# Kernel tuning notes

Hardware: AMD Instinct MI355X
Metric: run time of the kernel (lower is better)

Reference implementation:

```python
import jax, jax.numpy as jnp
import numpy as np
import math

V, D, H, F, L, S, B = 50257, 1024, 16, 4096, 4, 2048, 2
DK = D // H

def setup_inputs() -> dict:
    key = jax.random.key(0)
    ks = iter(jax.random.split(key, 32))
    std = 0.02
    def nrm(shape):
        return (std * jax.random.normal(next(ks), shape)).astype(jnp.float32)
    inp = {
        "x": jax.random.randint(next(ks), (B, S), 0, V, dtype=jnp.int32),
        "emb": nrm((V, D)),
        "ln1_g": jnp.ones((L, D), jnp.float32), "ln1_b": jnp.zeros((L, D), jnp.float32),
        "wq": nrm((L, D, D)), "wk": nrm((L, D, D)), "wv": nrm((L, D, D)), "wo": nrm((L, D, D)),
        "ln2_g": jnp.ones((L, D), jnp.float32), "ln2_b": jnp.zeros((L, D), jnp.float32),
        "w1": nrm((L, D, F)), "b1": jnp.zeros((L, F), jnp.float32),
        "w2": nrm((L, F, D)), "b2": jnp.zeros((L, D), jnp.float32),
        "lnf_g": jnp.ones((D,), jnp.float32), "lnf_b": jnp.zeros((D,), jnp.float32),
        "head_w": nrm((D, V)), "head_b": jnp.zeros((V,), jnp.float32),
    }
    return inp

def _layernorm(x, g, b, eps=1e-5):
    mu = jnp.mean(x, axis=-1, keepdims=True)
    var = jnp.var(x, axis=-1, keepdims=True)
    return (x - mu) * jax.lax.rsqrt(var + eps) * g + b

def _posenc(seq_len, d_model, dtype):
    pos = jnp.arange(seq_len, dtype=jnp.float32)[:, None]                  # [S,1]
    div = jnp.exp(jnp.arange(0, d_model, 2, dtype=jnp.float32) * (-math.log(10000.0) / d_model))
    ang = pos * div                                                        # [S,D/2]
    pe = jnp.stack([jnp.sin(ang), jnp.cos(ang)], axis=-1).reshape(seq_len, d_model)
    return pe.astype(dtype)

def reference(x, emb, ln1_g, ln1_b, wq, wk, wv, wo, ln2_g, ln2_b, w1, b1, w2, b2, lnf_g, lnf_b, head_w, head_b):
    b, s = x.shape
    h = emb[x] + _posenc(s, D, emb.dtype)[None]                            # [B,S,D]
    causal = jnp.tril(jnp.ones((s, s), dtype=bool))                       # True = keep
    scale = 1.0 / math.sqrt(DK)
    neg_inf = jnp.finfo(h.dtype).min
    for l in range(L):
        # --- attention sublayer ---
        hn = _layernorm(h, ln1_g[l], ln1_b[l])
        q = (hn @ wq[l]).reshape(b, s, H, DK)
        k = (hn @ wk[l]).reshape(b, s, H, DK)
        v = (hn @ wv[l]).reshape(b, s, H, DK)
        scores = jnp.einsum("bqhd,bkhd->bhqk", q, k) * scale
        scores = jnp.where(causal[None, None], scores, neg_inf)
        w = jax.nn.softmax(scores, axis=-1)
        attn = jnp.einsum("bhqk,bkhd->bqhd", w, v).reshape(b, s, D)
        h = h + attn @ wo[l]
        # --- FFN sublayer ---
        hn = _layernorm(h, ln2_g[l], ln2_b[l])
        h = h + jax.nn.relu(hn @ w1[l] + b1[l]) @ w2[l] + b2[l]
    h = _layernorm(h, lnf_g, lnf_b)
    logits = h @ head_w + head_b                                           # [B,S,V]
    return logits
```

## Files before the change

### kernel.cpp

```cpp
#include <hip/hip_runtime.h>
#include <math.h>

#define VOCAB 50257
#define VPAD  50432
#define DM    1024
#define NH    16
#define DKH   64
#define FF    4096
#define NL    4
#define SEQ   2048
#define BATCH 2
#define MROWS (BATCH*SEQ)

typedef __bf16 bf16_t;
typedef __bf16 bf16x8 __attribute__((ext_vector_type(8)));
typedef __bf16 bf16x4 __attribute__((ext_vector_type(4)));
typedef float  f32x4  __attribute__((ext_vector_type(4)));

typedef void as1_void __attribute__((address_space(1)));
typedef void as3_void __attribute__((address_space(3)));

__device__ __forceinline__ void gload_lds16(const void* g, void* l) {
  __builtin_amdgcn_global_load_lds((as1_void*)g, (as3_void*)l, 16, 0, 0);
}

__device__ __forceinline__ uint32_t lds_addr32(const void* p) {
  return (uint32_t)(uintptr_t)(as3_void*)p;
}

__device__ __forceinline__ bf16x8 dsr128(uint32_t addr) {
  bf16x8 v;
  asm volatile("ds_read_b128 %0, %1" : "=v"(v) : "v"(addr));
  return v;
}

#define FENCE asm volatile("" ::: "memory")
#define BAR() do { FENCE; __builtin_amdgcn_s_barrier(); FENCE; } while (0)
#define LGKM0_FENCE() do { \
  asm volatile("s_waitcnt lgkmcnt(0)" ::: "memory"); \
  __builtin_amdgcn_sched_barrier(0); \
} while (0)

__global__ __launch_bounds__(256) void embed_kernel(const int* __restrict__ x,
    const float* __restrict__ emb, float* __restrict__ h) {
  int row = blockIdx.x;
  int s = row & (SEQ - 1);
  int d = threadIdx.x * 4;
  const float* e = emb + (size_t)x[row] * DM + d;
  float4 v = *(const float4*)e;
  float vin[4] = {v.x, v.y, v.z, v.w};
  float out[4];
#pragma unroll
  for (int j = 0; j < 4; ++j) {
    int dd = d + j;
    int i = dd >> 1;
    float freq = expf(-0.017988946039016376f * (float)i);
    float ang = (float)s * freq;
    float pe = (dd & 1) ? cosf(ang) : sinf(ang);
    out[j] = vin[j] + pe;
  }
  *(float4*)(h + (size_t)row * DM + d) = make_float4(out[0], out[1], out[2], out[3]);
}

__global__ __launch_bounds__(256) void ln_kernel(const float* __restrict__ x,
    const float* __restrict__ g, const float* __restrict__ b, bf16_t* __restrict__ out) {
  int row = blockIdx.x;
  int tid = threadIdx.x, lane = tid & 63, wave = tid >> 6;
  const float* xr = x + (size_t)row * DM;
  float4 v = ((const float4*)xr)[tid];
  float s1 = v.x + v.y + v.z + v.w;
  float s2 = v.x * v.x + v.y * v.y + v.z * v.z + v.w * v.w;
#pragma unroll
  for (int d = 1; d < 64; d <<= 1) { s1 += __shfl_xor(s1, d); s2 += __shfl_xor(s2, d); }
  __shared__ float red[8];
  if (lane == 0) { red[wave] = s1; red[4 + wave] = s2; }
  __syncthreads();
  s1 = red[0] + red[1] + red[2] + red[3];
  s2 = red[4] + red[5] + red[6] + red[7];
  float mu = s1 * (1.0f / DM);
  float var = s2 * (1.0f / DM) - mu * mu;
  float rs = rsqrtf(var + 1e-5f);
  float4 gv = ((const float4*)g)[tid];
  float4 bv = ((const float4*)b)[tid];
  bf16x4 o;
  o[0] = (bf16_t)((v.x - mu) * rs * gv.x + bv.x);
  o[1] = (bf16_t)((v.y - mu) * rs * gv.y + bv.y);
  o[2] = (bf16_t)((v.z - mu) * rs * gv.z + bv.z);
  o[3] = (bf16_t)((v.w - mu) * rs * gv.w + bv.w);
  *(bf16x4*)(out + (size_t)row * DM + tid * 4) = o;
}

__global__ __launch_bounds__(256) void transpose_cast_kernel(const float* __restrict__ in,
    bf16_t* __restrict__ out, int K, int N, int Npad) {
  __shared__ float tile[32][33];
  int n0 = blockIdx.x * 32, k0 = blockIdx.y * 32;
  int tx = threadIdx.x & 31, ty = threadIdx.x >> 5;
#pragma unroll
  for (int kk = ty; kk < 32; kk += 8) {
    int n = n0 + tx;
    tile[kk][tx] = (n < N) ? in[(size_t)(k0 + kk) * N + n] : 0.f;
  }
  __syncthreads();
#pragma unroll
  for (int nn = ty; nn < 32; nn += 8) {
    out[(size_t)(n0 + nn) * K + k0 + tx] = (bf16_t)tile[tx][nn];
  }
}

__global__ __launch_bounds__(256) void wtrans_kernel(
    const float* __restrict__ wq, const float* __restrict__ wk,
    const float* __restrict__ wv, const float* __restrict__ wo,
    const float* __restrict__ w1, const float* __restrict__ w2,
    bf16_t* __restrict__ qkvT, bf16_t* __restrict__ woT,
    bf16_t* __restrict__ w1T, bf16_t* __restrict__ w2T) {
  int id = blockIdx.x;
  const float* src; bf16_t* dst; int K, N, tk, tn;
  if (id < 4096) {
    int m = id >> 10, tile_i = id & 1023;
    tk = tile_i >> 5; tn = tile_i & 31; K = 1024; N = 1024;
    src = (m == 0) ? wq : (m == 1) ? wk : (m == 2) ? wv : wo;
    dst = (m < 3) ? qkvT + (size_t)m * DM * DM : woT;
  } else if (id < 8192) {
    int tile_i = id - 4096;
    tk = tile_i >> 7; tn = tile_i & 127; K = 1024; N = 4096;
    src = w1; dst = w1T;
  } else {
    int tile_i = id - 8192;
    tk = tile_i >> 5; tn = tile_i & 31; K = 4096; N = 1024;
    src = w2; dst = w2T;
  }
  __shared__ float tile[32][33];
  int n0 = tn * 32, k0 = tk * 32;
  int tx = threadIdx.x & 31, ty = threadIdx.x >> 5;
#pragma unroll
  for (int kk = ty; kk < 32; kk += 8)
    tile[kk][tx] = src[(size_t)(k0 + kk) * N + n0 + tx];
  __syncthreads();
#pragma unroll
  for (int nn = ty; nn < 32; nn += 8)
    dst[(size_t)(n0 + nn) * K + k0 + tx] = (bf16_t)tile[tx][nn];
}

__global__ __launch_bounds__(256) void vtrans_kernel(const bf16_t* __restrict__ qkv,
    bf16_t* __restrict__ vT) {
  int sb = blockIdx.x, hh = blockIdx.y, bb = blockIdx.z;
  __shared__ bf16_t t[64][72];
  int tid = threadIdx.x;
  const bf16_t* src = qkv + ((size_t)bb * SEQ + sb * 64) * (3 * DM) + 2 * DM + hh * DKH;
#pragma unroll
  for (int c = 0; c < 2; ++c) {
    int u = c * 256 + tid;
    int s = u >> 3, d8 = u & 7;
    *(bf16x8*)&t[s][d8 * 8] = *(const bf16x8*)(src + (size_t)s * (3 * DM) + d8 * 8);
  }
  __syncthreads();
  bf16_t* dst = vT + ((size_t)(bb * NH + hh) * DKH) * SEQ + sb * 64;
#pragma unroll
  for (int c = 0; c < 2; ++c) {
    int u = c * 256 + tid;
    int dk = u >> 3, s8 = u & 7;
    bf16x8 v;
#pragma unroll
    for (int j = 0; j < 8; ++j) v[j] = t[s8 * 8 + j][dk];
    *(bf16x8*)(dst + (size_t)dk * SEQ + s8 * 8) = v;
  }
}

__global__ __launch_bounds__(256, 2) void gemm128_kernel(
    const bf16_t* __restrict__ A, const bf16_t* __restrict__ Bt, int K,
    const float* __restrict__ bias, const float* __restrict__ Rsd,
    float* Cf, bf16_t* Cb, int ldc, int Nvalid, int relu, int gridM, int gridN) {
  __shared__ __align__(16) bf16_t lds[32768];

  int nwg = gridM * gridN;
  int orig = blockIdx.x;
  int q = nwg >> 3, rr = nwg & 7;
  int xcd = orig & 7, idx = orig >> 3;
  int swz = (xcd < rr ? xcd * (q + 1) : rr * (q + 1) + (xcd - rr) * q) + idx;
  int bm = swz % gridM, bn = swz / gridM;
  int m0 = bm * 128, n0 = bn * 128;

  int tid = threadIdx.x, lane = tid & 63, wave = tid >> 6;
  int g = lane >> 4, r = lane & 15;
  int wr = wave >> 1, wc = wave & 1;

  f32x4 zero = {0.f, 0.f, 0.f, 0.f};
  f32x4 acc[4][4];
#pragma unroll
  for (int i = 0; i < 4; ++i)
#pragma unroll
    for (int j = 0; j < 4; ++j) acc[i][j] = zero;

  const bf16_t* Abase = A + (size_t)m0 * K;
  const bf16_t* Bbase = Bt + (size_t)n0 * K;
  int NT = K >> 6;

  uint32_t L0 = lds_addr32(lds);
  uint32_t aF = L0 + (uint32_t)((g * 128 + wr * 64 + r) * 16);
  uint32_t bF = L0 + 32768u + (uint32_t)((g * 128 + wc * 64 + r) * 16);

  auto stage = [&](int t) {
    int b = t & 1, k0 = t << 6;
    bf16_t* dA = lds + (size_t)b * 8192;
    bf16_t* dB = lds + 16384 + (size_t)b * 8192;
#pragma unroll
    for (int j = 0; j < 4; ++j) {
      int u = j * 256 + tid;
      int row = u & 127, k8 = u >> 7;
      gload_lds16(Abase + (size_t)row * K + k0 + k8 * 8, dA + (j * 256 + wave * 64) * 8);
    }
#pragma unroll
    for (int j = 0; j < 4; ++j) {
      int u = j * 256 + tid;
      int row = u & 127, k8 = u >> 7;
      gload_lds16(Bbase + (size_t)row * K + k0 + k8 * 8, dB + (j * 256 + wave * 64) * 8);
    }
  };

  stage(0);
  if (NT > 1) {
    stage(1);
    asm volatile("s_waitcnt vmcnt(8)" ::: "memory");
  } else {
    asm volatile("s_waitcnt vmcnt(0)" ::: "memory");
  }
  BAR();

  for (int t = 0; t < NT; ++t) {
    uint32_t boff = (uint32_t)((t & 1) << 14);
    bf16x8 af[4][2], bfr[4][2];
#pragma unroll
    for (int mr = 0; mr < 4; ++mr)
#pragma unroll
      for (int kk = 0; kk < 2; ++kk)
        af[mr][kk] = dsr128(aF + boff + (uint32_t)(kk * 8192 + mr * 256));
#pragma unroll
    for (int nr = 0; nr < 4; ++nr)
#pragma unroll
      for (int kk = 0; kk < 2; ++kk)
        bfr[nr][kk] = dsr128(bF + boff + (uint32_t)(kk * 8192 + nr * 256));
    LGKM0_FENCE();
    BAR();
    if (t + 2 < NT) stage(t + 2);
    __builtin_amdgcn_s_setprio(1);
#pragma unroll
    for (int mr = 0; mr < 4; ++mr)
#pragma unroll
      for (int nr = 0; nr < 4; ++nr) {
        acc[mr][nr] = __builtin_amdgcn_mfma_f32_16x16x32_bf16(af[mr][0], bfr[nr][0], acc[mr][nr], 0, 0, 0);
        acc[mr][nr] = __builtin_amdgcn_mfma_f32_16x16x32_bf16(af[mr][1], bfr[nr][1], acc[mr][nr], 0, 0, 0);
      }
    __builtin_amdgcn_s_setprio(0);
    __builtin_amdgcn_sched_barrier(0);
    if (t + 2 < NT) {
      asm volatile("s_waitcnt vmcnt(8)" ::: "memory");
    } else {
      asm volatile("s_waitcnt vmcnt(0)" ::: "memory");
    }
    BAR();
  }

#pragma unroll
  for (int mr = 0; mr < 4; ++mr) {
    int row = m0 + wr * 64 + mr * 16 + g * 4;
#pragma unroll
    for (int nr = 0; nr < 4; ++nr) {
      int col = n0 + wc * 64 + nr * 16 + r;
      if (col < Nvalid) {
        float bval = bias ? bias[col] : 0.f;
#pragma unroll
        for (int i = 0; i < 4; ++i) {
          float vv = acc[mr][nr][i] + bval;
          if (relu) vv = fmaxf(vv, 0.f);
          size_t idxo = (size_t)(row + i) * ldc + col;
          if (Rsd) vv += Rsd[idxo];
          if (Cf) Cf[idxo] = vv;
          if (Cb) Cb[idxo] = (bf16_t)vv;
        }
      }
    }
  }
}

__global__ __launch_bounds__(512, 2) void gemm256_kernel(
    const bf16_t* __restrict__ A, const bf16_t* __restrict__ Bt, int K,
    const float* __restrict__ bias, float* Cf, bf16_t* Cb,
    int ldc, int Nvalid, int relu, int gridM, int gridN) {
  __shared__ __align__(16) bf16_t lds[65536];

  int nwg = gridM * gridN;
  int orig = blockIdx.x;
  int q = nwg >> 3, rr = nwg & 7;
  int xcd = orig & 7, idx = orig >> 3;
  int swz = (xcd < rr ? xcd * (q + 1) : rr * (q + 1) + (xcd - rr) * q) + idx;
  int bm = swz % gridM, bn = swz / gridM;
  int m0 = bm * 256, n0 = bn * 256;

  int tid = threadIdx.x, lane = tid & 63, wave = tid >> 6;
  int g = lane >> 4, r = lane & 15;
  int wr = wave >> 2, wc = wave & 3;

  f32x4 zero = {0.f, 0.f, 0.f, 0.f};
  f32x4 acc[8][4];
#pragma unroll
  for (int i = 0; i < 8; ++i)
#pragma unroll
    for (int j = 0; j < 4; ++j) acc[i][j] = zero;

  const bf16_t* Ab = A + (size_t)m0 * K;
  const bf16_t* Bb = Bt + (size_t)n0 * K;
  int NT = K >> 6;

  uint32_t L0 = lds_addr32(lds);
  uint32_t laneOff = (uint32_t)(g * 2048 + r * 16);
  uint32_t aBase0 = L0 + ((uint32_t)wr << 14) + laneOff;
  uint32_t bBase0 = L0 + 65536u + ((uint32_t)(wc >> 1) << 14) + laneOff
                  + (uint32_t)((wc & 1) * 1024);

  auto stageA = [&](int t, int hh) {
    int b = t & 1, k0 = t << 6;
    const bf16_t* src = Ab + (size_t)(hh * 128) * K + k0;
    bf16_t* dst = lds + (size_t)(b * 2 + hh) * 8192;
#pragma unroll
    for (int j = 0; j < 2; ++j) {
      int u = j * 512 + tid;
      gload_lds16(src + (size_t)(u & 127) * K + (u >> 7) * 8, dst + (j * 512 + wave * 64) * 8);
    }
  };
  auto stageB = [&](int t, int hh) {
    int b = t & 1, k0 = t << 6;
    const bf16_t* src = Bb + (size_t)(hh * 128) * K + k0;
    bf16_t* dst = lds + 32768 + (size_t)(b * 2 + hh) * 8192;
#pragma unroll
    for (int j = 0; j < 2; ++j) {
      int u = j * 512 + tid;
      gload_lds16(src + (size_t)(u & 127) * K + (u >> 7) * 8, dst + (j * 512 + wave * 64) * 8);
    }
  };

  stageB(0, 0); stageB(0, 1); stageA(0, 0); stageA(0, 1);
  if (NT > 1) {
    stageB(1, 0); stageB(1, 1);
    asm volatile("s_waitcnt vmcnt(4)" ::: "memory");
  } else {
    asm volatile("s_waitcnt vmcnt(0)" ::: "memory");
  }
  BAR();

  for (int t = 0; t < NT; ++t) {
    uint32_t bsel = (uint32_t)((t & 1) << 15);
    uint32_t Aaddr = aBase0 + bsel;
    uint32_t Baddr = bBase0 + bsel;

    bf16x8 a0[4][2], a1[4][2], b01[2][2], b23[2][2];

#pragma unroll
    for (int mi = 0; mi < 4; ++mi)
#pragma unroll
      for (int kk = 0; kk < 2; ++kk)
        a0[mi][kk] = dsr128(Aaddr + (uint32_t)(kk * 8192 + mi * 256));
#pragma unroll
    for (int ni = 0; ni < 2; ++ni)
#pragma unroll
      for (int kk = 0; kk < 2; ++kk)
        b01[ni][kk] = dsr128(Baddr + (uint32_t)(kk * 8192 + ni * 256));
    if (t + 1 < NT) stageA(t + 1, 0);
    BAR();
    LGKM0_FENCE();
    __builtin_amdgcn_s_setprio(1);
#pragma unroll
    for (int mi = 0; mi < 4; ++mi)
#pragma unroll
      for (int ni = 0; ni < 2; ++ni)
#pragma unroll
        for (int kk = 0; kk < 2; ++kk)
          acc[mi][ni] = __builtin_amdgcn_mfma_f32_16x16x32_bf16(a0[mi][kk], b01[ni][kk], acc[mi][ni], 0, 0, 0);
    __builtin_amdgcn_s_setprio(0);
    __builtin_amdgcn_sched_barrier(0);
    BAR();

#pragma unroll
    for (int ni = 0; ni < 2; ++ni)
#pragma unroll
      for (int kk = 0; kk < 2; ++kk)
        b23[ni][kk] = dsr128(Baddr + (uint32_t)(kk * 8192 + (ni + 2) * 256));
    if (t + 1 < NT) stageA(t + 1, 1);
    BAR();
    LGKM0_FENCE();
    __builtin_amdgcn_s_setprio(1);
#pragma unroll
    for (int mi = 0; mi < 4; ++mi)
#pragma unroll
      for (int ni = 0; ni < 2; ++ni)
#pragma unroll
        for (int kk = 0; kk < 2; ++kk)
          acc[mi][ni + 2] = __builtin_amdgcn_mfma_f32_16x16x32_bf16(a0[mi][kk], b23[ni][kk], acc[mi][ni + 2], 0, 0, 0);
    __builtin_amdgcn_s_setprio(0);
    __builtin_amdgcn_sched_barrier(0);
    BAR();

#pragma unroll
    for (int mi = 0; mi < 4; ++mi)
#pragma unroll
      for (int kk = 0; kk < 2; ++kk)
        a1[mi][kk] = dsr128(Aaddr + (uint32_t)(kk * 8192 + (mi + 4) * 256));
    if (t + 2 < NT) stageB(t + 2, 0);
    BAR();
    LGKM0_FENCE();
    __builtin_amdgcn_s_setprio(1);
#pragma unroll
    for (int mi = 0; mi < 4; ++mi)
#pragma unroll
      for (int ni = 0; ni < 2; ++ni)
#pragma unroll
        for (int kk = 0; kk < 2; ++kk)
          acc[mi + 4][ni] = __builtin_amdgcn_mfma_f32_16x16x32_bf16(a1[mi][kk], b01[ni][kk], acc[mi + 4][ni], 0, 0, 0);
    __builtin_amdgcn_s_setprio(0);
    __builtin_amdgcn_sched_barrier(0);
    BAR();

    if (t + 2 < NT) stageB(t + 2, 1);
    __builtin_amdgcn_sched_barrier(0);
    __builtin_amdgcn_s_setprio(1);
#pragma unroll
    for (int mi = 0; mi < 4; ++mi)
#pragma unroll
      for (int ni = 0; ni < 2; ++ni)
#pragma unroll
        for (int kk = 0; kk < 2; ++kk)
          acc[mi + 4][ni + 2] = __builtin_amdgcn_mfma_f32_16x16x32_bf16(a1[mi][kk], b23[ni][kk], acc[mi + 4][ni + 2], 0, 0, 0);
    __builtin_amdgcn_s_setprio(0);
    __builtin_amdgcn_sched_barrier(0);
    if (t + 2 < NT) {
      asm volatile("s_waitcnt vmcnt(4)" ::: "memory");
    } else {
      asm volatile("s_waitcnt vmcnt(0)" ::: "memory");
    }
    BAR();
  }

#pragma unroll
  for (int mi = 0; mi < 8; ++mi) {
    int row = m0 + wr * 128 + mi * 16 + g * 4;
#pragma unroll
    for (int ni = 0; ni < 4; ++ni) {
      int col = n0 + wc * 64 + ni * 16 + r;
      if (col < Nvalid) {
        float bval = bias ? bias[col] : 0.f;
#pragma unroll
        for (int i = 0; i < 4; ++i) {
          float vv = acc[mi][ni][i] + bval;
          if (relu) vv = fmaxf(vv, 0.f);
          size_t idxo = (size_t)(row + i) * ldc + col;
          if (Cf) Cf[idxo] = vv;
          if (Cb) Cb[idxo] = (bf16_t)vv;
        }
      }
    }
  }
}

__global__ __launch_bounds__(512, 4) void gemmhd_kernel(
    const bf16_t* __restrict__ A, const bf16_t* __restrict__ Bt, int K,
    const float* __restrict__ bias, float* __restrict__ Cf,
    int ldc, int Nvalid, int gridM, int gridN) {
  __shared__ __align__(16) bf16_t lds[24576];

  int nwg = gridM * gridN;
  int orig = blockIdx.x;
  int q = nwg >> 3, rr = nwg & 7;
  int xcd = orig & 7, idx = orig >> 3;
  int swz = (xcd < rr ? xcd * (q + 1) : rr * (q + 1) + (xcd - rr) * q) + idx;
  int bm = swz % gridM, bn = swz / gridM;
  int m0 = bm * 128, n0 = bn * 256;

  int tid = threadIdx.x, lane = tid & 63, wave = tid >> 6;
  int g = lane >> 4, r = lane & 15;
  int wr = wave >> 2, wc = wave & 3;

  f32x4 zero = {0.f, 0.f, 0.f, 0.f};
  f32x4 acc[4][4];
#pragma unroll
  for (int i = 0; i < 4; ++i)
#pragma unroll
    for (int j = 0; j < 4; ++j) acc[i][j] = zero;

  const bf16_t* Abase = A + (size_t)m0 * K;
  const bf16_t* Bbase = Bt + (size_t)n0 * K;
  int NT = K >> 5;

  uint32_t L0 = lds_addr32(lds);
  uint32_t aF = L0 + (uint32_t)(g * 2048 + (wr * 64 + r) * 16);
  uint32_t bF = L0 + 16384u + (uint32_t)(g * 4096 + (wc * 64 + r) * 16);

  auto stage = [&](int t) {
    int b = t & 1, k0 = t << 5;
    bf16_t* dA = lds + (size_t)b * 4096;
    bf16_t* dB = lds + 8192 + (size_t)b * 8192;
    {
      int u = tid;
      int row = u & 127, k8 = u >> 7;
      gload_lds16(Abase + (size_t)row * K + k0 + k8 * 8, dA + (wave * 64) * 8);
    }
#pragma unroll
    for (int j = 0; j < 2; ++j) {
      int u = j * 512 + tid;
      int row = u & 255, k8 = u >> 8;
      gload_lds16(Bbase + (size_t)row * K + k0 + k8 * 8, dB + (j * 512 + wave * 64) * 8);
    }
  };

  stage(0);
  if (NT > 1) {
    stage(1);
    asm volatile("s_waitcnt vmcnt(3)" ::: "memory");
  } else {
    asm volatile("s_waitcnt vmcnt(0)" ::: "memory");
  }
  BAR();

  for (int t = 0; t < NT; ++t) {
    uint32_t aoff = (uint32_t)((t & 1) << 13);
    uint32_t boff = (uint32_t)((t & 1) << 14);
    bf16x8 af[4], bfr[4];
#pragma unroll
    for (int mr = 0; mr < 4; ++mr) af[mr] = dsr128(aF + aoff + (uint32_t)(mr * 256));
#pragma unroll
    for (int nr = 0; nr < 4; ++nr) bfr[nr] = dsr128(bF + boff + (uint32_t)(nr * 256));
    LGKM0_FENCE();
    BAR();
    if (t + 2 < NT) stage(t + 2);
    __builtin_amdgcn_s_setprio(1);
#pragma unroll
    for (int mr = 0; mr < 4; ++mr)
#pragma unroll
      for (int nr = 0; nr < 4; ++nr)
        acc[mr][nr] = __builtin_amdgcn_mfma_f32_16x16x32_bf16(af[mr], bfr[nr], acc[mr][nr], 0, 0, 0);
    __builtin_amdgcn_s_setprio(0);
    __builtin_amdgcn_sched_barrier(0);
    if (t + 2 < NT) {
      asm volatile("s_waitcnt vmcnt(3)" ::: "memory");
    } else {
      asm volatile("s_waitcnt vmcnt(0)" ::: "memory");
    }
    BAR();
  }

#pragma unroll
  for (int mr = 0; mr < 4; ++mr) {
    int row = m0 + wr * 64 + mr * 16 + g * 4;
#pragma unroll
    for (int nr = 0; nr < 4; ++nr) {
      int col = n0 + wc * 64 + nr * 16 + r;
      if (col < Nvalid) {
        float bval = bias ? bias[col] : 0.f;
#pragma unroll
        for (int i = 0; i < 4; ++i) {
          Cf[(size_t)(row + i) * ldc + col] = acc[mr][nr][i] + bval;
        }
      }
    }
  }
}

__global__ __launch_bounds__(512, 4) void attn_kernel(const bf16_t* __restrict__ Qg,
    const bf16_t* __restrict__ Kg, const bf16_t* __restrict__ vT, bf16_t* __restrict__ Og,
    int ldq) {
  int bq = (int)gridDim.x - 1 - (int)blockIdx.x;
  int hh = blockIdx.y, bb = blockIdx.z;
  int tid = threadIdx.x, lane = tid & 63, wave = tid >> 6;
  int g = lane >> 4, r = lane & 15;
  __shared__ __align__(16) bf16_t Kl[2][4096];
  __shared__ __align__(16) bf16_t Vl[2][4096];
  __shared__ __align__(16) bf16_t Pl[8][1024];

  size_t base = (size_t)bb * SEQ * ldq + hh * DKH;
  size_t vbase = ((size_t)(bb * NH + hh)) * DKH * SEQ;
  size_t baseO = (size_t)bb * SEQ * DM + hh * DKH;
  int q0 = bq * 128 + wave * 16;
  const bf16_t* qrowp = Qg + base + (size_t)(q0 + r) * ldq;
  bf16x8 qf0 = *(const bf16x8*)(qrowp + g * 8);
  bf16x8 qf1 = *(const bf16x8*)(qrowp + 32 + g * 8);
#pragma unroll
  for (int j = 0; j < 8; ++j) {
    qf0[j] = (bf16_t)((float)qf0[j] * 0.125f);
    qf1[j] = (bf16_t)((float)qf1[j] * 0.125f);
  }

  uint32_t KlA = lds_addr32(&Kl[0][0]);
  uint32_t VlA = lds_addr32(&Vl[0][0]);
  int slot0 = g ^ (r & 7), slot1 = (4 + g) ^ (r & 7);

  f32x4 zero = {0.f, 0.f, 0.f, 0.f};
  f32x4 accO[4];
#pragma unroll
  for (int dt = 0; dt < 4; ++dt) accO[dt] = zero;
  float m_i[4], l_i[4];
#pragma unroll
  for (int i = 0; i < 4; ++i) { m_i[i] = -1e30f; l_i[i] = 0.f; }

  int skv = tid >> 3, kslot = tid & 7, kdk8 = kslot ^ (skv & 7);
  int sdk = tid >> 3, vslot = tid & 7, vkv8 = vslot ^ (sdk & 7);
  const bf16_t* ksrc0 = Kg + base + (size_t)skv * ldq + kdk8 * 8;
  const bf16_t* vsrc0 = vT + vbase + (size_t)sdk * SEQ + vkv8 * 8;

  auto stage = [&](int kb) {
    int c = kb & 1;
    gload_lds16(ksrc0 + (size_t)(kb * 64) * ldq, &Kl[c][(wave * 64) * 8]);
    gload_lds16(vsrc0 + kb * 64, &Vl[c][(wave * 64) * 8]);
  };

  int nkb = 2 * bq + 2;
  stage(0); stage(1);
  asm volatile("s_waitcnt vmcnt(2)" ::: "memory");
  BAR();

  for (int kb = 0; kb < nkb; ++kb) {
    uint32_t koff = KlA + (uint32_t)((kb & 1) << 13);
    uint32_t voff = VlA + (uint32_t)((kb & 1) << 13);

    bf16x8 kf[4][2];
#pragma unroll
    for (int ct = 0; ct < 4; ++ct) {
      int kvrow = ct * 16 + r;
      kf[ct][0] = dsr128(koff + (uint32_t)((kvrow * 8 + slot0) * 16));
      kf[ct][1] = dsr128(koff + (uint32_t)((kvrow * 8 + slot1) * 16));
    }
    LGKM0_FENCE();
    f32x4 sc[4];
#pragma unroll
    for (int ct = 0; ct < 4; ++ct) {
      f32x4 s = zero;
      s = __builtin_amdgcn_mfma_f32_16x16x32_bf16(qf0, kf[ct][0], s, 0, 0, 0);
      s = __builtin_amdgcn_mfma_f32_16x16x32_bf16(qf1, kf[ct][1], s, 0, 0, 0);
      sc[ct] = s;
    }

    bool full = (kb * 64 + 63) <= q0;
#pragma unroll
    for (int i = 0; i < 4; ++i) {
      float mx = m_i[i];
      if (full) {
#pragma unroll
        for (int ct = 0; ct < 4; ++ct) mx = fmaxf(mx, sc[ct][i]);
      } else {
        int qglob = q0 + g * 4 + i;
#pragma unroll
        for (int ct = 0; ct < 4; ++ct) {
          int kglob = kb * 64 + ct * 16 + r;
          float s = (kglob <= qglob) ? sc[ct][i] : -1e30f;
          sc[ct][i] = s;
          mx = fmaxf(mx, s);
        }
      }
#pragma unroll
      for (int d = 1; d < 16; d <<= 1) mx = fmaxf(mx, __shfl_xor(mx, d));
      float scl = __expf(m_i[i] - mx);
      l_i[i] *= scl;
      m_i[i] = mx;
      float rsum = 0.f;
#pragma unroll
      for (int ct = 0; ct < 4; ++ct) {
        float p = __expf(sc[ct][i] - mx);
        sc[ct][i] = p;
        rsum += p;
      }
#pragma unroll
      for (int d = 1; d < 16; d <<= 1) rsum += __shfl_xor(rsum, d);
      l_i[i] += rsum;
#pragma unroll
      for (int dt = 0; dt < 4; ++dt) accO[dt][i] *= scl;
    }

#pragma unroll
    for (int ct = 0; ct < 4; ++ct) {
      int kcol = ct * 16 + r;
#pragma unroll
      for (int i = 0; i < 4; ++i)
        Pl[wave][((kcol >> 3) * 16 + g * 4 + i) * 8 + (kcol & 7)] = (bf16_t)sc[ct][i];
    }
    bf16x8 pa0 = *(const bf16x8*)&Pl[wave][((0 + g) * 16 + r) * 8];
    bf16x8 pa1 = *(const bf16x8*)&Pl[wave][((4 + g) * 16 + r) * 8];

    bf16x8 vb[4][2];
#pragma unroll
    for (int dt = 0; dt < 4; ++dt) {
      int dkrow = dt * 16 + r;
      vb[dt][0] = dsr128(voff + (uint32_t)((dkrow * 8 + slot0) * 16));
      vb[dt][1] = dsr128(voff + (uint32_t)((dkrow * 8 + slot1) * 16));
    }
    LGKM0_FENCE();
#pragma unroll
    for (int dt = 0; dt < 4; ++dt) {
      accO[dt] = __builtin_amdgcn_mfma_f32_16x16x32_bf16(pa0, vb[dt][0], accO[dt], 0, 0, 0);
      accO[dt] = __builtin_amdgcn_mfma_f32_16x16x32_bf16(pa1, vb[dt][1], accO[dt], 0, 0, 0);
    }

    BAR();
    if (kb + 2 < nkb) {
      stage(kb + 2);
      asm volatile("s_waitcnt vmcnt(2)" ::: "memory");
    } else {
      asm volatile("s_waitcnt vmcnt(0)" ::: "memory");
    }
    BAR();
  }

#pragma unroll
  for (int dt = 0; dt < 4; ++dt)
#pragma unroll
    for (int i = 0; i < 4; ++i) {
      int rowq = q0 + g * 4 + i;
      Og[baseO + (size_t)rowq * DM + dt * 16 + r] = (bf16_t)(accO[dt][i] / l_i[i]);
    }
}

static inline void launch_gemm256(const bf16_t* A, const bf16_t* Bt, int K,
    const float* bias, float* Cf, bf16_t* Cb, int ldc, int Nvalid, int relu,
    int M, int Npad, hipStream_t stream) {
  int gridM = M / 256, gridN = Npad / 256;
  gemm256_kernel<<<dim3(gridM * gridN), 512, 0, stream>>>(
      A, Bt, K, bias, Cf, Cb, ldc, Nvalid, relu, gridM, gridN);
}

static inline void launch_gemm128(const bf16_t* A, const bf16_t* Bt, int K,
    const float* bias, const float* Rsd, float* Cf, bf16_t* Cb,
    int ldc, int Nvalid, int relu, int M, int Npad, hipStream_t stream) {
  int gridM = M / 128, gridN = Npad / 128;
  gemm128_kernel<<<dim3(gridM * gridN), 256, 0, stream>>>(
      A, Bt, K, bias, Rsd, Cf, Cb, ldc, Nvalid, relu, gridM, gridN);
}

extern "C" void kernel_launch(void* const* d_in, const int* in_sizes, int n_in,
                              void* d_out, int out_size, void* d_ws, size_t ws_size,
                              hipStream_t stream) {
  const int*   x      = (const int*)d_in[0];
  const float* emb    = (const float*)d_in[1];
  const float* ln1_g  = (const float*)d_in[2];
  const float* ln1_b  = (const float*)d_in[3];
  const float* wq     = (const float*)d_in[4];
  const float* wk     = (const float*)d_in[5];
  const float* wv     = (const float*)d_in[6];
  const float* wo     = (const float*)d_in[7];
  const float* ln2_g  = (const float*)d_in[8];
  const float* ln2_b  = (const float*)d_in[9];
  const float* w1     = (const float*)d_in[10];
  const float* b1     = (const float*)d_in[11];
  const float* w2     = (const float*)d_in[12];
  const float* b2     = (const float*)d_in[13];
  const float* lnf_g  = (const float*)d_in[14];
  const float* lnf_b  = (const float*)d_in[15];
  const float* head_w = (const float*)d_in[16];
  const float* head_b = (const float*)d_in[17];
  float* out = (float*)d_out;

  char* ws = (char*)d_ws;
  size_t off = 0;
  auto alloc = [&](size_t bytes) -> void* {
    void* p = ws + off;
    off += (bytes + 255) & ~(size_t)255;
    return p;
  };
  float*  h     = (float*)alloc((size_t)MROWS * DM * 4);
  bf16_t* hn    = (bf16_t*)alloc((size_t)MROWS * DM * 2);
  bf16_t* qkv   = (bf16_t*)alloc((size_t)MROWS * 3 * DM * 2);
  bf16_t* atb   = (bf16_t*)alloc((size_t)MROWS * DM * 2);
  bf16_t* ffn1  = (bf16_t*)alloc((size_t)MROWS * FF * 2);
  bf16_t* vTb   = (bf16_t*)alloc((size_t)BATCH * NH * DKH * SEQ * 2);
  bf16_t* headT = (bf16_t*)alloc((size_t)VPAD * DM * 2);
  bf16_t* wqkvT = headT;
  bf16_t* woT   = headT + (size_t)3 * DM * DM;
  bf16_t* w1T   = headT + (size_t)4 * DM * DM;
  bf16_t* w2T   = headT + (size_t)4 * DM * DM + (size_t)DM * FF;

  embed_kernel<<<MROWS, 256, 0, stream>>>(x, emb, h);

  for (int l = 0; l < NL; ++l) {
    ln_kernel<<<MROWS, 256, 0, stream>>>(h, ln1_g + l * DM, ln1_b + l * DM, hn);

    wtrans_kernel<<<12288, 256, 0, stream>>>(
        wq + (size_t)l * DM * DM, wk + (size_t)l * DM * DM, wv + (size_t)l * DM * DM,
        wo + (size_t)l * DM * DM, w1 + (size_t)l * DM * FF, w2 + (size_t)l * FF * DM,
        wqkvT, woT, w1T, w2T);

    launch_gemm256(hn, wqkvT, DM, nullptr, nullptr, qkv, 3 * DM, 3 * DM, 0,
                   MROWS, 3 * DM, stream);

    vtrans_kernel<<<dim3(SEQ / 64, NH, BATCH), 256, 0, stream>>>(qkv, vTb);
    attn_kernel<<<dim3(SEQ / 128, NH, BATCH), 512, 0, stream>>>(
        qkv, qkv + DM, vTb, atb, 3 * DM);

    launch_gemm128(atb, woT, DM, nullptr, h, h, nullptr, DM, DM, 0, MROWS, DM, stream);

    ln_kernel<<<MROWS, 256, 0, stream>>>(h, ln2_g + l * DM, ln2_b + l * DM, hn);

    launch_gemm256(hn, w1T, DM, b1 + (size_t)l * FF, nullptr, ffn1, FF, FF, 1,
                   MROWS, FF, stream);

    launch_gemm128(ffn1, w2T, FF, b2 + (size_t)l * DM, h, h, nullptr, DM, DM, 0,
                   MROWS, DM, stream);
  }

  ln_kernel<<<MROWS, 256, 0, stream>>>(h, lnf_g, lnf_b, hn);
  transpose_cast_kernel<<<dim3(VPAD / 32, DM / 32), 256, 0, stream>>>(
      head_w, headT, DM, VOCAB, VPAD);
  gemmhd_kernel<<<dim3((MROWS / 128) * (VPAD / 256)), 512, 0, stream>>>(
      hn, headT, DM, head_b, out, VOCAB, VOCAB, MROWS / 128, VPAD / 256);
}
```

Before: 2.473 ms.

## Retile vocab-head GEMM to 256x256 with K=64 stages; lazily rescale attention softmax

The output-projection GEMM now uses 256x256 tiles with a 64-wide K step and a double-buffered 128 KB LDS footprint. Each wave does 8x4 MFMA tiles over two k-subslices, which raises operand reuse per byte loaded and halves the number of barriers per K. In exchange, occupancy drops to about one workgroup per CU and register pressure rises. Separately, flash attention skips the running-max update and accumulator rescale when no row's block max exceeds the current max by more than 8. This accepts larger unnormalised exponentials in exchange for fewer exps and multiplies.

```diff
diff --git a/kernel.cpp b/kernel.cpp
--- a/kernel.cpp
+++ b/kernel.cpp
@@ -460,11 +460,11 @@
   }
 }
 
-__global__ __launch_bounds__(512, 4) void gemmhd_kernel(
+__global__ __launch_bounds__(512, 2) void gemm256v2_kernel(
     const bf16_t* __restrict__ A, const bf16_t* __restrict__ Bt, int K,
     const float* __restrict__ bias, float* __restrict__ Cf,
     int ldc, int Nvalid, int gridM, int gridN) {
-  __shared__ __align__(16) bf16_t lds[24576];
+  __shared__ __align__(16) bf16_t lds[65536];
 
   int nwg = gridM * gridN;
   int orig = blockIdx.x;
@@ -472,74 +472,82 @@
   int xcd = orig & 7, idx = orig >> 3;
   int swz = (xcd < rr ? xcd * (q + 1) : rr * (q + 1) + (xcd - rr) * q) + idx;
   int bm = swz % gridM, bn = swz / gridM;
-  int m0 = bm * 128, n0 = bn * 256;
+  int m0 = bm * 256, n0 = bn * 256;
 
   int tid = threadIdx.x, lane = tid & 63, wave = tid >> 6;
   int g = lane >> 4, r = lane & 15;
   int wr = wave >> 2, wc = wave & 3;
 
   f32x4 zero = {0.f, 0.f, 0.f, 0.f};
-  f32x4 acc[4][4];
-#pragma unroll
-  for (int i = 0; i < 4; ++i)
+  f32x4 acc[8][4];
+#pragma unroll
+  for (int i = 0; i < 8; ++i)
 #pragma unroll
     for (int j = 0; j < 4; ++j) acc[i][j] = zero;
 
-  const bf16_t* Abase = A + (size_t)m0 * K;
-  const bf16_t* Bbase = Bt + (size_t)n0 * K;
-  int NT = K >> 5;
+  const bf16_t* Ab = A + (size_t)m0 * K;
+  const bf16_t* Bb = Bt + (size_t)n0 * K;
+  int NT = K >> 6;
 
   uint32_t L0 = lds_addr32(lds);
-  uint32_t aF = L0 + (uint32_t)(g * 2048 + (wr * 64 + r) * 16);
-  uint32_t bF = L0 + 16384u + (uint32_t)(g * 4096 + (wc * 64 + r) * 16);
+  uint32_t aF = L0 + (uint32_t)(g * 4096 + (wr * 128 + r) * 16);
+  uint32_t bF = L0 + 65536u + (uint32_t)(g * 4096 + (wc * 64 + r) * 16);
 
   auto stage = [&](int t) {
-    int b = t & 1, k0 = t << 5;
-    bf16_t* dA = lds + (size_t)b * 4096;
-    bf16_t* dB = lds + 8192 + (size_t)b * 8192;
-    {
-      int u = tid;
-      int row = u & 127, k8 = u >> 7;
-      gload_lds16(Abase + (size_t)row * K + k0 + k8 * 8, dA + (wave * 64) * 8);
-    }
-#pragma unroll
-    for (int j = 0; j < 2; ++j) {
+    int b = t & 1, k0 = t << 6;
+    bf16_t* dA = lds + (size_t)b * 16384;
+    bf16_t* dB = lds + 32768 + (size_t)b * 16384;
+#pragma unroll
+    for (int j = 0; j < 4; ++j) {
       int u = j * 512 + tid;
       int row = u & 255, k8 = u >> 8;
-      gload_lds16(Bbase + (size_t)row * K + k0 + k8 * 8, dB + (j * 512 + wave * 64) * 8);
+      gload_lds16(Ab + (size_t)row * K + k0 + k8 * 8, dA + (j * 512 + wave * 64) * 8);
+    }
+#pragma unroll
+    for (int j = 0; j < 4; ++j) {
+      int u = j * 512 + tid;
+      int row = u & 255, k8 = u >> 8;
+      gload_lds16(Bb + (size_t)row * K + k0 + k8 * 8, dB + (j * 512 + wave * 64) * 8);
     }
   };
 
   stage(0);
   if (NT > 1) {
     stage(1);
-    asm volatile("s_waitcnt vmcnt(3)" ::: "memory");
+    asm volatile("s_waitcnt vmcnt(8)" ::: "memory");
   } else {
     asm volatile("s_waitcnt vmcnt(0)" ::: "memory");
   }
   BAR();
 
   for (int t = 0; t < NT; ++t) {
-    uint32_t aoff = (uint32_t)((t & 1) << 13);
-    uint32_t boff = (uint32_t)((t & 1) << 14);
-    bf16x8 af[4], bfr[4];
-#pragma unroll
-    for (int mr = 0; mr < 4; ++mr) af[mr] = dsr128(aF + aoff + (uint32_t)(mr * 256));
-#pragma unroll
-    for (int nr = 0; nr < 4; ++nr) bfr[nr] = dsr128(bF + boff + (uint32_t)(nr * 256));
+    uint32_t bsel = (uint32_t)((t & 1) << 15);
+    bf16x8 af[8][2], bfr[4][2];
+#pragma unroll
+    for (int mi = 0; mi < 8; ++mi)
+#pragma unroll
+      for (int kk = 0; kk < 2; ++kk)
+        af[mi][kk] = dsr128(aF + bsel + (uint32_t)(kk * 16384 + mi * 256));
+#pragma unroll
+    for (int ni = 0; ni < 4; ++ni)
+#pragma unroll
+      for (int kk = 0; kk < 2; ++kk)
+        bfr[ni][kk] = dsr128(bF + bsel + (uint32_t)(kk * 16384 + ni * 256));
     LGKM0_FENCE();
     BAR();
     if (t + 2 < NT) stage(t + 2);
     __builtin_amdgcn_s_setprio(1);
 #pragma unroll
-    for (int mr = 0; mr < 4; ++mr)
-#pragma unroll
-      for (int nr = 0; nr < 4; ++nr)
-        acc[mr][nr] = __builtin_amdgcn_mfma_f32_16x16x32_bf16(af[mr], bfr[nr], acc[mr][nr], 0, 0, 0);
+    for (int mi = 0; mi < 8; ++mi)
+#pragma unroll
+      for (int ni = 0; ni < 4; ++ni)
+#pragma unroll
+        for (int kk = 0; kk < 2; ++kk)
+          acc[mi][ni] = __builtin_amdgcn_mfma_f32_16x16x32_bf16(af[mi][kk], bfr[ni][kk], acc[mi][ni], 0, 0, 0);
     __builtin_amdgcn_s_setprio(0);
     __builtin_amdgcn_sched_barrier(0);
     if (t + 2 < NT) {
-      asm volatile("s_waitcnt vmcnt(3)" ::: "memory");
+      asm volatile("s_waitcnt vmcnt(8)" ::: "memory");
     } else {
       asm volatile("s_waitcnt vmcnt(0)" ::: "memory");
     }
@@ -547,17 +555,16 @@
   }
 
 #pragma unroll
-  for (int mr = 0; mr < 4; ++mr) {
-    int row = m0 + wr * 64 + mr * 16 + g * 4;
-#pragma unroll
-    for (int nr = 0; nr < 4; ++nr) {
-      int col = n0 + wc * 64 + nr * 16 + r;
+  for (int mi = 0; mi < 8; ++mi) {
+    int row = m0 + wr * 128 + mi * 16 + g * 4;
+#pragma unroll
+    for (int ni = 0; ni < 4; ++ni) {
+      int col = n0 + wc * 64 + ni * 16 + r;
       if (col < Nvalid) {
         float bval = bias ? bias[col] : 0.f;
 #pragma unroll
-        for (int i = 0; i < 4; ++i) {
-          Cf[(size_t)(row + i) * ldc + col] = acc[mr][nr][i] + bval;
-        }
+        for (int i = 0; i < 4; ++i)
+          Cf[(size_t)(row + i) * ldc + col] = acc[mi][ni][i] + bval;
       }
     }
   }
@@ -637,9 +644,10 @@
     }
 
     bool full = (kb * 64 + 63) <= q0;
+    float tmx[4];
 #pragma unroll
     for (int i = 0; i < 4; ++i) {
-      float mx = m_i[i];
+      float mx = -1e30f;
       if (full) {
 #pragma unroll
         for (int ct = 0; ct < 4; ++ct) mx = fmaxf(mx, sc[ct][i]);
@@ -655,21 +663,31 @@
       }
 #pragma unroll
       for (int d = 1; d < 16; d <<= 1) mx = fmaxf(mx, __shfl_xor(mx, d));
-      float scl = __expf(m_i[i] - mx);
-      l_i[i] *= scl;
-      m_i[i] = mx;
+      tmx[i] = mx;
+    }
+
+    bool skip = __all(tmx[0] <= m_i[0] + 8.f && tmx[1] <= m_i[1] + 8.f &&
+                      tmx[2] <= m_i[2] + 8.f && tmx[3] <= m_i[3] + 8.f);
+#pragma unroll
+    for (int i = 0; i < 4; ++i) {
+      if (!skip) {
+        float mnew = fmaxf(m_i[i], tmx[i]);
+        float scl = __expf(m_i[i] - mnew);
+        l_i[i] *= scl;
+        m_i[i] = mnew;
+#pragma unroll
+        for (int dt = 0; dt < 4; ++dt) accO[dt][i] *= scl;
+      }
       float rsum = 0.f;
 #pragma unroll
       for (int ct = 0; ct < 4; ++ct) {
-        float p = __expf(sc[ct][i] - mx);
+        float p = __expf(sc[ct][i] - m_i[i]);
         sc[ct][i] = p;
         rsum += p;
       }
 #pragma unroll
       for (int d = 1; d < 16; d <<= 1) rsum += __shfl_xor(rsum, d);
       l_i[i] += rsum;
-#pragma unroll
-      for (int dt = 0; dt < 4; ++dt) accO[dt][i] *= scl;
     }
 
 #pragma unroll
@@ -804,6 +822,6 @@
   ln_kernel<<<MROWS, 256, 0, stream>>>(h, lnf_g, lnf_b, hn);
   transpose_cast_kernel<<<dim3(VPAD / 32, DM / 32), 256, 0, stream>>>(
       head_w, headT, DM, VOCAB, VPAD);
-  gemmhd_kernel<<<dim3((MROWS / 128) * (VPAD / 256)), 512, 0, stream>>>(
-      hn, headT, DM, head_b, out, VOCAB, VOCAB, MROWS / 128, VPAD / 256);
-}
+  gemm256v2_kernel<<<dim3((MROWS / 256) * (VPAD / 256)), 512, 0, stream>>>(
+      hn, headT, DM, head_b, out, VOCAB, VOCAB, MROWS / 256, VPAD / 256);
+}
```

Result: no change. 2.459 ms (-0.6%).
